# Optimization experiments

Measured on AMD Instinct MI355X. Metric: run time of the kernel, lower is better.

## Reference

```python
import jax, jax.numpy as jnp
import numpy as np

H, W = 480, 640
NUM_SEM = 12      # len(stuff_labels)+1
NUM_INS = 16      # number of detected instances
NUM_THING = 9     # len(thing_labels)+1
NUM_ITER = 3
GAMMA_SEM = 3.0
GAMMA_INS = 3.0
ALPHA_SEM = 3.0
BETA_SEM = 0.15
ALPHA_INS = 3.0
BETA_INS = 0.15
R_BIL = 2         # bilateral truncation radius


def _gauss1d(sigma):
    r = int(np.ceil(2.0 * sigma))
    x = np.arange(-r, r + 1, dtype=np.float32)
    k = np.exp(-0.5 * (x / sigma) ** 2)
    k /= k.sum()
    return jnp.asarray(k)


def _sep_blur(q, k):
    # normalized Gaussian spatial filter, separable depthwise conv. q: (C,H,W)
    C = q.shape[0]
    K = k.shape[0]
    p = K // 2
    x = q[None]  # (1,C,H,W)
    kh = jnp.broadcast_to(k.reshape(1, 1, K, 1), (C, 1, K, 1))
    x = jax.lax.conv_general_dilated(x, kh, (1, 1), [(p, p), (0, 0)], feature_group_count=C)
    kw = jnp.broadcast_to(k.reshape(1, 1, 1, K), (C, 1, 1, K))
    x = jax.lax.conv_general_dilated(x, kw, (1, 1), [(0, 0), (p, p)], feature_group_count=C)
    return x[0]


def _bilateral(q, image, alpha, beta, R):
    # truncated-window bilateral (joint spatial/color Gaussian), normalized per pixel
    C, Hh, Ww = q.shape
    Ip = jnp.pad(image, ((0, 0), (R, R), (R, R)), mode='edge')
    qp = jnp.pad(q, ((0, 0), (R, R), (R, R)), mode='edge')
    num = jnp.zeros_like(q)
    den = jnp.zeros((Hh, Ww), q.dtype)
    inv2a2 = 1.0 / (2.0 * alpha * alpha)
    inv2b2 = 1.0 / (2.0 * beta * beta)
    for dy in range(2 * R + 1):
        for dx in range(2 * R + 1):
            Ish = P = Ip[:, dy:dy + Hh, dx:dx + Ww]
            cd = jnp.sum((image - Ish) ** 2, axis=0)          # color distance (H,W)
            sd = float((dy - R) ** 2 + (dx - R) ** 2)          # spatial distance
            w = jnp.exp(-sd * inv2a2 - cd * inv2b2)
            num = num + w[None] * qp[:, dy:dy + Hh, dx:dx + Ww]
            den = den + w
    return num / den[None]


def _compat(q, M):
    # torch.mm(M.t(), q.view(Cin,-1)).view(Cout,H,W)
    return jnp.einsum('io,ihw->ohw', M, q)


def setup_inputs() -> dict:
    key = jax.random.key(0)
    ks = jax.random.split(key, 6)
    return {
        'image': jax.random.uniform(ks[0], (3, H, W), jnp.float32),
        'semantic_logits': jax.random.normal(ks[1], (NUM_SEM, H, W), jnp.float32),
        'instance_logits': jax.random.normal(ks[2], (NUM_INS, H, W), jnp.float32),
        'instance_cls_labels': jax.random.randint(ks[3], (NUM_INS,), 0, NUM_THING),
        'sem_spatial_w': 3.0 * jnp.ones((NUM_SEM,), jnp.float32),
        'sem_bilateral_w': 5.0 * jnp.ones((NUM_SEM,), jnp.float32),
        'sem_compat': jnp.eye(NUM_SEM, dtype=jnp.float32),
        'ins_spatial_w': 3.0 * jnp.ones((NUM_THING,), jnp.float32),
        'ins_bilateral_w': 3.0 * jnp.ones((NUM_THING,), jnp.float32),
        'cross_ins_sem': 0.1 * jax.random.normal(ks[4], (NUM_THING, NUM_SEM), jnp.float32),
        'cross_sem_ins': 0.1 * jax.random.normal(ks[5], (NUM_THING, NUM_SEM), jnp.float32),
    }


def reference(image, semantic_logits, instance_logits, instance_cls_labels,
              sem_spatial_w, sem_bilateral_w, sem_compat,
              ins_spatial_w, ins_bilateral_w, cross_ins_sem, cross_sem_ins):
    k_sem = _gauss1d(GAMMA_SEM)
    k_ins = _gauss1d(GAMMA_INS)
    sem_q = jax.nn.softmax(semantic_logits, axis=0)
    ins_q = jax.nn.softmax(instance_logits, axis=0)
    sw = ins_spatial_w[instance_cls_labels][:, None, None]      # (NI,1,1)
    bw = ins_bilateral_w[instance_cls_labels][:, None, None]
    M_is = cross_ins_sem[instance_cls_labels]                   # (NI, NUM_SEM)
    M_si = cross_sem_ins[instance_cls_labels].T                 # (NUM_SEM, NI)
    for _ in range(NUM_ITER):
        sp_sem = sem_spatial_w[:, None, None] * _sep_blur(sem_q, k_sem)
        bl_sem = sem_bilateral_w[:, None, None] * _bilateral(sem_q, image, ALPHA_SEM, BETA_SEM, R_BIL)
        tmp_sem = semantic_logits + _compat(sp_sem + bl_sem, sem_compat)
        sp_ins = sw * _sep_blur(ins_q, k_ins)
        bl_ins = bw * _bilateral(ins_q, image, ALPHA_INS, BETA_INS, R_BIL)
        tmp_ins = instance_logits + sp_ins + bl_ins
        tmp_sem_new = tmp_sem + _compat(jax.nn.softmax(tmp_ins, axis=0), M_is)
        tmp_ins_new = tmp_ins + _compat(jax.nn.softmax(tmp_sem, axis=0), M_si)
        sem_q = jax.nn.softmax(tmp_sem_new, axis=0)
        ins_q = jax.nn.softmax(tmp_ins_new, axis=0)
    return sem_q, ins_q
```

## Files before the change

kernel.cpp:

```cpp
#include <hip/hip_runtime.h>

#define HH   480
#define WW   640
#define HWP  (HH*WW)
#define NSEM 12
#define NINS 16
#define NCH  28

typedef _Float16 f16_t;

union P32 { f16_t h[32]; int4 v[4]; };
union I4H8 { int4 v; f16_t h[8]; };

__device__ __forceinline__ void gauss13(float k[13]) {
    float s = 0.f;
#pragma unroll
    for (int j = 0; j < 13; ++j) {
        float xx = (float)(j - 6);
        float v  = __expf(-(xx * xx) * (1.f / 18.f));
        k[j] = v; s += v;
    }
    float inv = 1.f / s;
#pragma unroll
    for (int j = 0; j < 13; ++j) k[j] *= inv;
}

template <int N>
__device__ __forceinline__ void softmaxN(const float* __restrict__ in, float* __restrict__ out) {
    float m = in[0];
#pragma unroll
    for (int i = 1; i < N; ++i) m = fmaxf(m, in[i]);
    float s = 0.f;
#pragma unroll
    for (int i = 0; i < N; ++i) { float e = __expf(in[i] - m); out[i] = e; s += e; }
    float inv = 1.f / s;
#pragma unroll
    for (int i = 0; i < N; ++i) out[i] *= inv;
}

__global__ __launch_bounds__(256) void init_kernel(const float* __restrict__ semL,
                                                   const float* __restrict__ insL,
                                                   int4* __restrict__ qcl4,
                                                   f16_t* __restrict__ qpm) {
    int p = blockIdx.x * 256 + threadIdx.x;
    float v[NINS], o[NINS];
    P32 pk;
#pragma unroll
    for (int i = 0; i < 32; ++i) pk.h[i] = (f16_t)0.f;
#pragma unroll
    for (int i = 0; i < NSEM; ++i) v[i] = semL[i * HWP + p];
    softmaxN<NSEM>(v, o);
#pragma unroll
    for (int i = 0; i < NSEM; ++i) { f16_t h = (f16_t)o[i]; pk.h[i] = h; qpm[i * HWP + p] = h; }
#pragma unroll
    for (int i = 0; i < NINS; ++i) v[i] = insL[i * HWP + p];
    softmaxN<NINS>(v, o);
#pragma unroll
    for (int i = 0; i < NINS; ++i) { f16_t h = (f16_t)o[i]; pk.h[NSEM + i] = h; qpm[(NSEM + i) * HWP + p] = h; }
#pragma unroll
    for (int j = 0; j < 4; ++j) qcl4[p * 4 + j] = pk.v[j];
}

#define BTW 64
#define BTH 32
#define RAWW 80
#define RAWH 44
__global__ __launch_bounds__(256) void blur_fused_kernel(const f16_t* __restrict__ in,
                                                         f16_t* __restrict__ out) {
    __shared__ float raw[RAWH * RAWW];
    __shared__ float hb[RAWH * BTW];
    const int t  = threadIdx.x;
    const int x0 = blockIdx.x * BTW;
    const int y0 = blockIdx.y * BTH;
    const int c  = blockIdx.z;
    const f16_t* __restrict__ plane = in + (size_t)c * HWP;

    float k[13]; gauss13(k);

    for (int idx = t; idx < RAWH * 10; idx += 256) {
        int row = idx / 10, g = idx - row * 10;
        int gy = y0 - 6 + row;
        int gx8 = x0 - 8 + g * 8;
        float4 lo = {0.f,0.f,0.f,0.f}, hi = {0.f,0.f,0.f,0.f};
        if (gy >= 0 && gy < HH && gx8 >= 0 && gx8 <= WW - 8) {
            I4H8 u; u.v = *(const int4*)&plane[gy * WW + gx8];
            lo.x = (float)u.h[0]; lo.y = (float)u.h[1]; lo.z = (float)u.h[2]; lo.w = (float)u.h[3];
            hi.x = (float)u.h[4]; hi.y = (float)u.h[5]; hi.z = (float)u.h[6]; hi.w = (float)u.h[7];
        }
        *(float4*)&raw[row * RAWW + g * 8]     = lo;
        *(float4*)&raw[row * RAWW + g * 8 + 4] = hi;
    }
    __syncthreads();

    for (int idx = t; idx < RAWH * 16; idx += 256) {
        int row = idx >> 4, xg = idx & 15;
        const float* rp = &raw[row * RAWW + xg * 4];
        float f[20];
#pragma unroll
        for (int q4 = 0; q4 < 5; ++q4) {
            float4 v = *(const float4*)&rp[q4 * 4];
            f[q4*4+0]=v.x; f[q4*4+1]=v.y; f[q4*4+2]=v.z; f[q4*4+3]=v.w;
        }
        float4 o;
        float* op = &o.x;
#pragma unroll
        for (int j = 0; j < 4; ++j) {
            float a = 0.f;
#pragma unroll
            for (int i = 0; i < 13; ++i) a = fmaf(k[i], f[j + 2 + i], a);
            op[j] = a;
        }
        *(float4*)&hb[row * BTW + xg * 4] = o;
    }
    __syncthreads();

    for (int idx = t; idx < BTW * 8; idx += 256) {
        int tx = idx & 63, yg = idx >> 6;
        float hh[16];
#pragma unroll
        for (int i = 0; i < 16; ++i) hh[i] = hb[(yg * 4 + i) * BTW + tx];
#pragma unroll
        for (int j = 0; j < 4; ++j) {
            float a = 0.f;
#pragma unroll
            for (int i = 0; i < 13; ++i) a = fmaf(k[i], hh[j + i], a);
            out[(size_t)c * HWP + (y0 + yg * 4 + j) * WW + (x0 + tx)] = (f16_t)a;
        }
    }
}

#define TTW 32
#define TTH 8
#define TWW (TTW + 4)
#define TWH (TTH + 4)
#define TWN (TWW * TWH)

template <bool LAST>
__global__ __launch_bounds__(256) void tail_kernel(const int4* __restrict__ qcl4,
                                                   const f16_t* __restrict__ sp,
                                                   const float* __restrict__ img,
                                                   const float* __restrict__ semL,
                                                   const float* __restrict__ insL,
                                                   const float* __restrict__ sem_sw,
                                                   const float* __restrict__ sem_bw,
                                                   const float* __restrict__ sem_compat,
                                                   const float* __restrict__ ins_sw,
                                                   const float* __restrict__ ins_bw,
                                                   const int*   __restrict__ labels,
                                                   const float* __restrict__ cross_is,
                                                   const float* __restrict__ cross_si,
                                                   int4* __restrict__ qclo4,
                                                   f16_t* __restrict__ qpmo,
                                                   float* __restrict__ dout) {
    __shared__ int4  lq4[TWN * 5];
    __shared__ float limg[3 * TWN];
    __shared__ float sC[NSEM * NSEM];
    __shared__ float sMis[NINS * NSEM];
    __shared__ float sMsi[NINS * NSEM];
    __shared__ float sws[NSEM], sbs[NSEM], swi[NINS], sbi[NINS];

    const int t  = threadIdx.x;
    const int tx = t & 31;
    const int ty = t >> 5;
    const int x0 = blockIdx.x * TTW;
    const int y0 = blockIdx.y * TTH;
    const int p  = (y0 + ty) * WW + (x0 + tx);

    if (t < NSEM * NSEM) sC[t] = sem_compat[t];
    if (t < NINS * NSEM) {
        int i = t / NSEM, o = t - i * NSEM;
        sMis[t] = cross_is[labels[i] * NSEM + o];
        sMsi[t] = cross_si[labels[i] * NSEM + o];
    }
    if (t < NSEM) { sws[t] = sem_sw[t]; sbs[t] = sem_bw[t]; }
    if (t < NINS) { int l = labels[t]; swi[t] = ins_sw[l]; sbi[t] = ins_bw[l]; }

#pragma unroll
    for (int j = 0; j < 7; ++j) {
        int idx = t + j * 256;
        if (idx < TWN * 4) {
            int e = idx >> 2, grp = idx & 3;
            int ly = e / TWW, lx = e - ly * TWW;
            int gy = min(max(y0 - 2 + ly, 0), HH - 1);
            int gx = min(max(x0 - 2 + lx, 0), WW - 1);
            lq4[e * 5 + grp] = qcl4[(gy * WW + gx) * 4 + grp];
        }
    }
    for (int idx = t; idx < 3 * TWN; idx += 256) {
        int cc  = idx / TWN;
        int rem = idx - cc * TWN;
        int ly  = rem / TWW, lx = rem - ly * TWW;
        int gy  = min(max(y0 - 2 + ly, 0), HH - 1);
        int gx  = min(max(x0 - 2 + lx, 0), WW - 1);
        limg[idx] = img[(size_t)cc * HWP + gy * WW + gx];
    }
    __syncthreads();

    float wnr[25];
    {
        const int wc = (ty + 2) * TWW + (tx + 2);
        float i0 = limg[wc], i1 = limg[TWN + wc], i2 = limg[2 * TWN + wc];
        float den = 0.f;
        int d = 0;
#pragma unroll
        for (int dy = 0; dy < 5; ++dy) {
#pragma unroll
            for (int dx = 0; dx < 5; ++dx) {
                int nb = (ty + dy) * TWW + (tx + dx);
                float d0 = limg[nb] - i0;
                float d1 = limg[TWN + nb] - i1;
                float d2 = limg[2 * TWN + nb] - i2;
                float cd = d0 * d0 + d1 * d1 + d2 * d2;
                float sd = (float)((dy - 2) * (dy - 2) + (dx - 2) * (dx - 2));
                float wv = __expf(-sd * (1.f / 18.f) - cd * (1.f / 0.045f));
                wnr[d++] = wv; den += wv;
            }
        }
        float inv = 1.f / den;
#pragma unroll
        for (int j = 0; j < 25; ++j) wnr[j] *= inv;
    }

    float bl[NCH];
#pragma unroll
    for (int c = 0; c < NCH; ++c) bl[c] = 0.f;
#pragma unroll
    for (int dy = 0; dy < 5; ++dy) {
        int rb = ((ty + dy) * TWW + tx) * 5;
#pragma unroll
        for (int dx = 0; dx < 5; ++dx) {
            float w = wnr[dy * 5 + dx];
            int e5 = rb + dx * 5;
#pragma unroll
            for (int grp = 0; grp < 4; ++grp) {
                I4H8 u; u.v = lq4[e5 + grp];
                int lim = (grp == 3) ? 4 : 8;
#pragma unroll
                for (int i = 0; i < 8; ++i) {
                    if (i < lim)
                        bl[grp * 8 + i] = fmaf((float)u.h[i], w, bl[grp * 8 + i]);
                }
            }
        }
    }

    float comb[NSEM];
#pragma unroll
    for (int i = 0; i < NSEM; ++i)
        comb[i] = sws[i] * (float)sp[i * HWP + p] + sbs[i] * bl[i];
    float ts[NSEM];
#pragma unroll
    for (int o = 0; o < NSEM; ++o) {
        float a = semL[o * HWP + p];
#pragma unroll
        for (int i = 0; i < NSEM; ++i) a = fmaf(sC[i * NSEM + o], comb[i], a);
        ts[o] = a;
    }
    float ti[NINS];
#pragma unroll
    for (int i = 0; i < NINS; ++i)
        ti[i] = insL[i * HWP + p] + swi[i] * (float)sp[(NSEM + i) * HWP + p] + sbi[i] * bl[NSEM + i];

    float sIns[NINS], sSem[NSEM];
    softmaxN<NINS>(ti, sIns);
    softmaxN<NSEM>(ts, sSem);

    float nts[NSEM];
#pragma unroll
    for (int o = 0; o < NSEM; ++o) {
        float a = ts[o];
#pragma unroll
        for (int i = 0; i < NINS; ++i) a = fmaf(sMis[i * NSEM + o], sIns[i], a);
        nts[o] = a;
    }
    float nti[NINS];
#pragma unroll
    for (int o = 0; o < NINS; ++o) {
        float a = ti[o];
#pragma unroll
        for (int i = 0; i < NSEM; ++i) a = fmaf(sMsi[o * NSEM + i], sSem[i], a);
        nti[o] = a;
    }

    float oq1[NSEM], oq2[NINS];
    softmaxN<NSEM>(nts, oq1);
    softmaxN<NINS>(nti, oq2);

    if (LAST) {
#pragma unroll
        for (int i = 0; i < NSEM; ++i) dout[i * HWP + p] = oq1[i];
#pragma unroll
        for (int i = 0; i < NINS; ++i) dout[(NSEM + i) * HWP + p] = oq2[i];
    } else {
        P32 pk;
#pragma unroll
        for (int i = 0; i < 32; ++i) pk.h[i] = (f16_t)0.f;
#pragma unroll
        for (int i = 0; i < NSEM; ++i) { f16_t h = (f16_t)oq1[i]; pk.h[i] = h; qpmo[i * HWP + p] = h; }
#pragma unroll
        for (int i = 0; i < NINS; ++i) { f16_t h = (f16_t)oq2[i]; pk.h[NSEM + i] = h; qpmo[(NSEM + i) * HWP + p] = h; }
#pragma unroll
        for (int j = 0; j < 4; ++j) qclo4[p * 4 + j] = pk.v[j];
    }
}

extern "C" void kernel_launch(void* const* d_in, const int* in_sizes, int n_in,
                              void* d_out, int out_size, void* d_ws, size_t ws_size,
                              hipStream_t stream) {
    const float* image      = (const float*)d_in[0];
    const float* semL       = (const float*)d_in[1];
    const float* insL       = (const float*)d_in[2];
    const int*   labels     = (const int*)  d_in[3];
    const float* sem_sw     = (const float*)d_in[4];
    const float* sem_bw     = (const float*)d_in[5];
    const float* sem_compat = (const float*)d_in[6];
    const float* ins_sw     = (const float*)d_in[7];
    const float* ins_bw     = (const float*)d_in[8];
    const float* cross_is   = (const float*)d_in[9];
    const float* cross_si   = (const float*)d_in[10];

    char* ws = (char*)d_ws;
    int4*  qclA = (int4*)ws;                                    ws += (size_t)HWP * 64;
    int4*  qclB = (int4*)ws;                                    ws += (size_t)HWP * 64;
    f16_t* qpmA = (f16_t*)ws;                                   ws += (size_t)NCH * HWP * 2;
    f16_t* qpmB = (f16_t*)ws;                                   ws += (size_t)NCH * HWP * 2;
    f16_t* sp   = (f16_t*)ws;

    const int PIX_BLOCKS = HWP / 256;
    init_kernel<<<PIX_BLOCKS, 256, 0, stream>>>(semL, insL, qclA, qpmA);

    dim3 bgrid(WW / BTW, HH / BTH, NCH);
    dim3 tgrid(WW / TTW, HH / TTH);

    blur_fused_kernel<<<bgrid, 256, 0, stream>>>(qpmA, sp);
    tail_kernel<false><<<tgrid, 256, 0, stream>>>(qclA, sp, image, semL, insL,
                                                  sem_sw, sem_bw, sem_compat,
                                                  ins_sw, ins_bw, labels,
                                                  cross_is, cross_si, qclB, qpmB, nullptr);
    blur_fused_kernel<<<bgrid, 256, 0, stream>>>(qpmB, sp);
    tail_kernel<false><<<tgrid, 256, 0, stream>>>(qclB, sp, image, semL, insL,
                                                  sem_sw, sem_bw, sem_compat,
                                                  ins_sw, ins_bw, labels,
                                                  cross_is, cross_si, qclA, qpmA, nullptr);
    blur_fused_kernel<<<bgrid, 256, 0, stream>>>(qpmA, sp);
    tail_kernel<true><<<tgrid, 256, 0, stream>>>(qclA, sp, image, semL, insL,
                                                 sem_sw, sem_bw, sem_compat,
                                                 ins_sw, ins_bw, labels,
                                                 cross_is, cross_si, nullptr, nullptr, (float*)d_out);
}
```

Before: 315.1 us.

## Cache logits in fp16, vectorize vertical blur, shrink tail shared-memory footprint

The init kernel now writes fp16 copies of the semantic and instance logits, and the three tail passes read those instead of fp32, which halves that traffic. The vertical blur pass is rewritten so each thread produces a 4-wide by 2-row patch with float4 LDS reads and 8-byte global stores. The tail kernel's shared-memory halo drops the unused padding of the 32-slot packed layout (3 int4 plus 1 int2 per pixel instead of 5 int4), and launch bounds request 5 blocks per CU to raise occupancy. The logits lose precision in fp16, and the occupancy hint may force register spills.

```diff
diff --git a/kernel.cpp b/kernel.cpp
--- a/kernel.cpp
+++ b/kernel.cpp
@@ -11,6 +11,8 @@
 
 union P32 { f16_t h[32]; int4 v[4]; };
 union I4H8 { int4 v; f16_t h[8]; };
+union I2H4 { int2 v; f16_t h[4]; };
+union H4I2 { f16_t h[4]; int2 v; };
 
 __device__ __forceinline__ void gauss13(float k[13]) {
     float s = 0.f;
@@ -41,19 +43,21 @@
 __global__ __launch_bounds__(256) void init_kernel(const float* __restrict__ semL,
                                                    const float* __restrict__ insL,
                                                    int4* __restrict__ qcl4,
-                                                   f16_t* __restrict__ qpm) {
+                                                   f16_t* __restrict__ qpm,
+                                                   f16_t* __restrict__ semLh,
+                                                   f16_t* __restrict__ insLh) {
     int p = blockIdx.x * 256 + threadIdx.x;
     float v[NINS], o[NINS];
     P32 pk;
 #pragma unroll
     for (int i = 0; i < 32; ++i) pk.h[i] = (f16_t)0.f;
 #pragma unroll
-    for (int i = 0; i < NSEM; ++i) v[i] = semL[i * HWP + p];
+    for (int i = 0; i < NSEM; ++i) { v[i] = semL[i * HWP + p]; semLh[i * HWP + p] = (f16_t)v[i]; }
     softmaxN<NSEM>(v, o);
 #pragma unroll
     for (int i = 0; i < NSEM; ++i) { f16_t h = (f16_t)o[i]; pk.h[i] = h; qpm[i * HWP + p] = h; }
 #pragma unroll
-    for (int i = 0; i < NINS; ++i) v[i] = insL[i * HWP + p];
+    for (int i = 0; i < NINS; ++i) { v[i] = insL[i * HWP + p]; insLh[i * HWP + p] = (f16_t)v[i]; }
     softmaxN<NINS>(v, o);
 #pragma unroll
     for (int i = 0; i < NINS; ++i) { f16_t h = (f16_t)o[i]; pk.h[NSEM + i] = h; qpm[(NSEM + i) * HWP + p] = h; }
@@ -114,17 +118,25 @@
     }
     __syncthreads();
 
-    for (int idx = t; idx < BTW * 8; idx += 256) {
-        int tx = idx & 63, yg = idx >> 6;
-        float hh[16];
-#pragma unroll
-        for (int i = 0; i < 16; ++i) hh[i] = hb[(yg * 4 + i) * BTW + tx];
-#pragma unroll
-        for (int j = 0; j < 4; ++j) {
-            float a = 0.f;
-#pragma unroll
-            for (int i = 0; i < 13; ++i) a = fmaf(k[i], hh[j + i], a);
-            out[(size_t)c * HWP + (y0 + yg * 4 + j) * WW + (x0 + tx)] = (f16_t)a;
+    {
+        const int xg = t & 15;
+        const int yg = t >> 4;
+        float4 r[14];
+#pragma unroll
+        for (int i = 0; i < 14; ++i)
+            r[i] = *(const float4*)&hb[(yg * 2 + i) * BTW + xg * 4];
+#pragma unroll
+        for (int j = 0; j < 2; ++j) {
+            float a0 = 0.f, a1 = 0.f, a2 = 0.f, a3 = 0.f;
+#pragma unroll
+            for (int i = 0; i < 13; ++i) {
+                float4 v = r[j + i];
+                a0 = fmaf(k[i], v.x, a0); a1 = fmaf(k[i], v.y, a1);
+                a2 = fmaf(k[i], v.z, a2); a3 = fmaf(k[i], v.w, a3);
+            }
+            H4I2 s;
+            s.h[0] = (f16_t)a0; s.h[1] = (f16_t)a1; s.h[2] = (f16_t)a2; s.h[3] = (f16_t)a3;
+            *(int2*)&out[(size_t)c * HWP + (y0 + yg * 2 + j) * WW + (x0 + xg * 4)] = s.v;
         }
     }
 }
@@ -136,23 +148,24 @@
 #define TWN (TWW * TWH)
 
 template <bool LAST>
-__global__ __launch_bounds__(256) void tail_kernel(const int4* __restrict__ qcl4,
-                                                   const f16_t* __restrict__ sp,
-                                                   const float* __restrict__ img,
-                                                   const float* __restrict__ semL,
-                                                   const float* __restrict__ insL,
-                                                   const float* __restrict__ sem_sw,
-                                                   const float* __restrict__ sem_bw,
-                                                   const float* __restrict__ sem_compat,
-                                                   const float* __restrict__ ins_sw,
-                                                   const float* __restrict__ ins_bw,
-                                                   const int*   __restrict__ labels,
-                                                   const float* __restrict__ cross_is,
-                                                   const float* __restrict__ cross_si,
-                                                   int4* __restrict__ qclo4,
-                                                   f16_t* __restrict__ qpmo,
-                                                   float* __restrict__ dout) {
-    __shared__ int4  lq4[TWN * 5];
+__global__ __launch_bounds__(256, 5) void tail_kernel(const int4* __restrict__ qcl4,
+                                                      const f16_t* __restrict__ sp,
+                                                      const float* __restrict__ img,
+                                                      const f16_t* __restrict__ semLh,
+                                                      const f16_t* __restrict__ insLh,
+                                                      const float* __restrict__ sem_sw,
+                                                      const float* __restrict__ sem_bw,
+                                                      const float* __restrict__ sem_compat,
+                                                      const float* __restrict__ ins_sw,
+                                                      const float* __restrict__ ins_bw,
+                                                      const int*   __restrict__ labels,
+                                                      const float* __restrict__ cross_is,
+                                                      const float* __restrict__ cross_si,
+                                                      int4* __restrict__ qclo4,
+                                                      f16_t* __restrict__ qpmo,
+                                                      float* __restrict__ dout) {
+    __shared__ int4  lqA[TWN * 3];
+    __shared__ int2  lqB[TWN];
     __shared__ float limg[3 * TWN];
     __shared__ float sC[NSEM * NSEM];
     __shared__ float sMis[NINS * NSEM];
@@ -176,14 +189,24 @@
     if (t < NINS) { int l = labels[t]; swi[t] = ins_sw[l]; sbi[t] = ins_bw[l]; }
 
 #pragma unroll
-    for (int j = 0; j < 7; ++j) {
+    for (int j = 0; j < 6; ++j) {
         int idx = t + j * 256;
-        if (idx < TWN * 4) {
-            int e = idx >> 2, grp = idx & 3;
+        if (idx < TWN * 3) {
+            int e = idx / 3, s = idx - e * 3;
             int ly = e / TWW, lx = e - ly * TWW;
             int gy = min(max(y0 - 2 + ly, 0), HH - 1);
             int gx = min(max(x0 - 2 + lx, 0), WW - 1);
-            lq4[e * 5 + grp] = qcl4[(gy * WW + gx) * 4 + grp];
+            lqA[idx] = qcl4[(gy * WW + gx) * 4 + s];
+        }
+    }
+#pragma unroll
+    for (int j = 0; j < 2; ++j) {
+        int e = t + j * 256;
+        if (e < TWN) {
+            int ly = e / TWW, lx = e - ly * TWW;
+            int gy = min(max(y0 - 2 + ly, 0), HH - 1);
+            int gx = min(max(x0 - 2 + lx, 0), WW - 1);
+            lqB[e] = ((const int2*)qcl4)[(gy * WW + gx) * 8 + 6];
         }
     }
     for (int idx = t; idx < 3 * TWN; idx += 256) {
@@ -226,21 +249,22 @@
     for (int c = 0; c < NCH; ++c) bl[c] = 0.f;
 #pragma unroll
     for (int dy = 0; dy < 5; ++dy) {
-        int rb = ((ty + dy) * TWW + tx) * 5;
+        int rb = (ty + dy) * TWW + tx;
 #pragma unroll
         for (int dx = 0; dx < 5; ++dx) {
             float w = wnr[dy * 5 + dx];
-            int e5 = rb + dx * 5;
-#pragma unroll
-            for (int grp = 0; grp < 4; ++grp) {
-                I4H8 u; u.v = lq4[e5 + grp];
-                int lim = (grp == 3) ? 4 : 8;
-#pragma unroll
-                for (int i = 0; i < 8; ++i) {
-                    if (i < lim)
-                        bl[grp * 8 + i] = fmaf((float)u.h[i], w, bl[grp * 8 + i]);
-                }
+            int e = rb + dx;
+#pragma unroll
+            for (int s = 0; s < 3; ++s) {
+                I4H8 u; u.v = lqA[e * 3 + s];
+#pragma unroll
+                for (int i = 0; i < 8; ++i)
+                    bl[s * 8 + i] = fmaf((float)u.h[i], w, bl[s * 8 + i]);
             }
+            I2H4 ub; ub.v = lqB[e];
+#pragma unroll
+            for (int i = 0; i < 4; ++i)
+                bl[24 + i] = fmaf((float)ub.h[i], w, bl[24 + i]);
         }
     }
 
@@ -251,7 +275,7 @@
     float ts[NSEM];
 #pragma unroll
     for (int o = 0; o < NSEM; ++o) {
-        float a = semL[o * HWP + p];
+        float a = (float)semLh[o * HWP + p];
 #pragma unroll
         for (int i = 0; i < NSEM; ++i) a = fmaf(sC[i * NSEM + o], comb[i], a);
         ts[o] = a;
@@ -259,7 +283,7 @@
     float ti[NINS];
 #pragma unroll
     for (int i = 0; i < NINS; ++i)
-        ti[i] = insL[i * HWP + p] + swi[i] * (float)sp[(NSEM + i) * HWP + p] + sbi[i] * bl[NSEM + i];
+        ti[i] = (float)insLh[i * HWP + p] + swi[i] * (float)sp[(NSEM + i) * HWP + p] + sbi[i] * bl[NSEM + i];
 
     float sIns[NINS], sSem[NSEM];
     softmaxN<NINS>(ti, sIns);
@@ -320,30 +344,32 @@
     const float* cross_si   = (const float*)d_in[10];
 
     char* ws = (char*)d_ws;
-    int4*  qclA = (int4*)ws;                                    ws += (size_t)HWP * 64;
-    int4*  qclB = (int4*)ws;                                    ws += (size_t)HWP * 64;
-    f16_t* qpmA = (f16_t*)ws;                                   ws += (size_t)NCH * HWP * 2;
-    f16_t* qpmB = (f16_t*)ws;                                   ws += (size_t)NCH * HWP * 2;
-    f16_t* sp   = (f16_t*)ws;
+    int4*  qclA  = (int4*)ws;                                   ws += (size_t)HWP * 64;
+    int4*  qclB  = (int4*)ws;                                   ws += (size_t)HWP * 64;
+    f16_t* qpmA  = (f16_t*)ws;                                  ws += (size_t)NCH * HWP * 2;
+    f16_t* qpmB  = (f16_t*)ws;                                  ws += (size_t)NCH * HWP * 2;
+    f16_t* sp    = (f16_t*)ws;                                  ws += (size_t)NCH * HWP * 2;
+    f16_t* semLh = (f16_t*)ws;                                  ws += (size_t)NSEM * HWP * 2;
+    f16_t* insLh = (f16_t*)ws;
 
     const int PIX_BLOCKS = HWP / 256;
-    init_kernel<<<PIX_BLOCKS, 256, 0, stream>>>(semL, insL, qclA, qpmA);
+    init_kernel<<<PIX_BLOCKS, 256, 0, stream>>>(semL, insL, qclA, qpmA, semLh, insLh);
 
     dim3 bgrid(WW / BTW, HH / BTH, NCH);
     dim3 tgrid(WW / TTW, HH / TTH);
 
     blur_fused_kernel<<<bgrid, 256, 0, stream>>>(qpmA, sp);
-    tail_kernel<false><<<tgrid, 256, 0, stream>>>(qclA, sp, image, semL, insL,
+    tail_kernel<false><<<tgrid, 256, 0, stream>>>(qclA, sp, image, semLh, insLh,
                                                   sem_sw, sem_bw, sem_compat,
                                                   ins_sw, ins_bw, labels,
                                                   cross_is, cross_si, qclB, qpmB, nullptr);
     blur_fused_kernel<<<bgrid, 256, 0, stream>>>(qpmB, sp);
-    tail_kernel<false><<<tgrid, 256, 0, stream>>>(qclB, sp, image, semL, insL,
+    tail_kernel<false><<<tgrid, 256, 0, stream>>>(qclB, sp, image, semLh, insLh,
                                                   sem_sw, sem_bw, sem_compat,
                                                   ins_sw, ins_bw, labels,
                                                   cross_is, cross_si, qclA, qpmA, nullptr);
     blur_fused_kernel<<<bgrid, 256, 0, stream>>>(qpmA, sp);
-    tail_kernel<true><<<tgrid, 256, 0, stream>>>(qclA, sp, image, semL, insL,
+    tail_kernel<true><<<tgrid, 256, 0, stream>>>(qclA, sp, image, semLh, insLh,
                                                  sem_sw, sem_bw, sem_compat,
                                                  ins_sw, ins_bw, labels,
                                                  cross_is, cross_si, nullptr, nullptr, (float*)d_out);
```

New measurement: 280.6 us. 1.12x faster.
